# Performance work log

Measured on AMD Instinct MI355X. Metric: run time of the kernel, lower is better.

Reference implementation:

```python
import jax, jax.numpy as jnp
import numpy as np
import math

B, DIM, H, W = 4, 96, 64, 64
DIM3 = DIM * 3
DSTATE = 16

def _dwconv(x, w, b):
    # x: (B, d, L); torch Conv1d(k=4, pad=3, groups=d) then slice [:L] == left-pad 3
    y = jax.lax.conv_general_dilated(x, w, (1,), [(3, 0)],
                                     dimension_numbers=('NCH', 'OIH', 'NCH'),
                                     feature_group_count=x.shape[1])
    return y + b[None, :, None]

def _ln(x, g, b):
    m = jnp.mean(x, -1, keepdims=True)
    v = jnp.var(x, -1, keepdims=True)
    return (x - m) * jax.lax.rsqrt(v + 1e-5) * g + b

def _selective_scan(u, delta, A, Bs, Cs, D, z, delta_bias):
    # u, delta, z: (B, d, L); A: (d, N); Bs, Cs: (B, N, L)
    delta = jax.nn.softplus(delta + delta_bias[None, :, None])
    dT, uT = jnp.moveaxis(delta, 2, 0), jnp.moveaxis(u, 2, 0)   # (L, B, d)
    BT, CT = jnp.moveaxis(Bs, 2, 0), jnp.moveaxis(Cs, 2, 0)     # (L, B, N)
    h0 = jnp.zeros((u.shape[0], A.shape[0], A.shape[1]), u.dtype)
    def step(h, inp):
        d_t, u_t, b_t, c_t = inp
        h = jnp.exp(d_t[..., None] * A) * h + (d_t * u_t)[..., None] * b_t[:, None, :]
        return h, jnp.einsum('bdn,bn->bd', h, c_t)
    _, ys = jax.lax.scan(step, h0, (dT, uT, BT, CT))
    y = jnp.moveaxis(ys, 0, 2) + D[None, :, None] * u
    return y * jax.nn.silu(z)

def _sss(x, z_anchor, in_w, conv_w, conv_b, x_w, dt_w, dt_b, Alog, Dp, out_w):
    Bb, C, Hh, Ww = x.shape
    L = Hh * Ww
    r = dt_w.shape[0]
    xf = x.reshape(Bb, C, L).transpose(0, 2, 1) + z_anchor[:, None, :]
    x_in, z_gate = jnp.split(xf @ in_w, 2, axis=-1)
    xc = jax.nn.silu(_dwconv(x_in.transpose(0, 2, 1), conv_w, conv_b))  # (B, di, L)
    xdbl = xc.transpose(0, 2, 1) @ x_w
    dt, Bs, Cs = jnp.split(xdbl, [r, r + DSTATE], axis=-1)
    y = _selective_scan(xc, (dt @ dt_w).transpose(0, 2, 1), -jnp.exp(Alog),
                        Bs.transpose(0, 2, 1), Cs.transpose(0, 2, 1), Dp,
                        z_gate.transpose(0, 2, 1), dt_b)
    return (y.transpose(0, 2, 1) @ out_w).transpose(0, 2, 1).reshape(Bb, C, Hh, Ww)

def _sts(x, K, Q, in_w, conv_w, conv_b, kln_g, kln_b, k_w, k_b, qln_g, qln_b, q_w, q_b,
         dtbc_w, dt_w, dt_b, gate_w, gate_b, Alog, Dp, out_w):
    Bb, C, Hh, Ww = x.shape
    L = Hh * Ww
    r = dt_w.shape[0]
    xf = x.reshape(Bb, C, L).transpose(0, 2, 1)
    xc = jax.nn.silu(_dwconv((xf @ in_w).transpose(0, 2, 1), conv_w, conv_b))  # (B, di, L)
    x_t = xc.transpose(0, 2, 1)
    Kf = K.reshape(Bb, C, L).transpose(0, 2, 1)
    Qf = Q.reshape(Bb, C, L).transpose(0, 2, 1)
    K_p = jax.nn.silu(_ln(Kf, kln_g, kln_b) @ k_w + k_b)
    Q_p = jax.nn.silu(_ln(Qf, qln_g, qln_b) @ q_w + q_b)
    xdbl = jnp.concatenate([x_t, K_p], -1) @ dtbc_w
    dt, Bs, Cs = jnp.split(xdbl, [r, r + DSTATE], axis=-1)
    z_g = (jnp.concatenate([x_t, Q_p], -1) @ gate_w + gate_b).transpose(0, 2, 1)
    y = _selective_scan(xc, (dt @ dt_w).transpose(0, 2, 1), -jnp.exp(Alog),
                        Bs.transpose(0, 2, 1), Cs.transpose(0, 2, 1), Dp, z_g, dt_b)
    return (y.transpose(0, 2, 1) @ out_w).transpose(0, 2, 1).reshape(Bb, C, Hh, Ww)

def setup_inputs():
    key = jax.random.key(0)
    ks = iter(jax.random.split(key, 64))
    def nrm(shape, s=0.02):
        return jax.random.normal(next(ks), shape, jnp.float32) * s
    di, di3 = DIM * 2, DIM3 * 2
    r, r3 = math.ceil(DIM / 16), math.ceil(DIM3 / 16)
    Alog = jnp.log(jnp.tile(jnp.arange(1.0, DSTATE + 1.0, dtype=jnp.float32), (di, 1)))
    Alog3 = jnp.log(jnp.tile(jnp.arange(1.0, DSTATE + 1.0, dtype=jnp.float32), (di3, 1)))
    return dict(
        m_ll=jax.random.normal(next(ks), (B, DIM, H, W), jnp.float32),
        m_high=jax.random.normal(next(ks), (B, DIM3, H, W), jnp.float32),
        z=jax.random.normal(next(ks), (B, DIM), jnp.float32),
        K=jax.random.normal(next(ks), (B, DIM3, H, W), jnp.float32),
        Q=jax.random.normal(next(ks), (B, DIM3, H, W), jnp.float32),
        s_in_w=nrm((DIM, 2 * di)), s_conv_w=nrm((di, 1, 4), 0.2), s_conv_b=nrm((di,)),
        s_x_w=nrm((di, r + 2 * DSTATE)), s_dt_w=nrm((r, di)), s_dt_b=nrm((di,)),
        s_Alog=Alog, s_D=jnp.ones((di,), jnp.float32), s_out_w=nrm((di, DIM)),
        t_in_w=nrm((DIM3, di3)), t_conv_w=nrm((di3, 1, 4), 0.2), t_conv_b=nrm((di3,)),
        t_kln_g=jnp.ones((DIM3,), jnp.float32), t_kln_b=jnp.zeros((DIM3,), jnp.float32),
        t_k_w=nrm((DIM3, di3)), t_k_b=nrm((di3,)),
        t_qln_g=jnp.ones((DIM3,), jnp.float32), t_qln_b=jnp.zeros((DIM3,), jnp.float32),
        t_q_w=nrm((DIM3, di3)), t_q_b=nrm((di3,)),
        t_dtbc_w=nrm((2 * di3, r3 + 2 * DSTATE)), t_dt_w=nrm((r3, di3)), t_dt_b=nrm((di3,)),
        t_gate_w=nrm((2 * di3, di3)), t_gate_b=nrm((di3,)),
        t_Alog=Alog3, t_D=jnp.ones((di3,), jnp.float32), t_out_w=nrm((di3, DIM3)),
    )

def reference(m_ll, m_high, z, K, Q,
              s_in_w, s_conv_w, s_conv_b, s_x_w, s_dt_w, s_dt_b, s_Alog, s_D, s_out_w,
              t_in_w, t_conv_w, t_conv_b, t_kln_g, t_kln_b, t_k_w, t_k_b,
              t_qln_g, t_qln_b, t_q_w, t_q_b, t_dtbc_w, t_dt_w, t_dt_b,
              t_gate_w, t_gate_b, t_Alog, t_D, t_out_w):
    o1 = m_ll + _sss(m_ll, z, s_in_w, s_conv_w, s_conv_b, s_x_w, s_dt_w, s_dt_b, s_Alog, s_D, s_out_w)
    o2 = m_high + _sts(m_high, K, Q, t_in_w, t_conv_w, t_conv_b, t_kln_g, t_kln_b, t_k_w, t_k_b,
                       t_qln_g, t_qln_b, t_q_w, t_q_b, t_dtbc_w, t_dt_w, t_dt_b,
                       t_gate_w, t_gate_b, t_Alog, t_D, t_out_w)
    return (o1, o2)
```

## Files before the change

### kernel.cpp

```cpp
#include <hip/hip_runtime.h>
#include <math.h>

#define L 4096

typedef unsigned short u16;
typedef float f32x4 __attribute__((ext_vector_type(4)));
typedef short s16x8 __attribute__((ext_vector_type(8)));
typedef __attribute__((address_space(3))) unsigned int lds_u32;
typedef __attribute__((address_space(1))) unsigned int glb_u32;

__device__ __forceinline__ float softplus_f(float x) {
  return fmaxf(x, 0.f) + log1pf(__expf(-fabsf(x)));
}
__device__ __forceinline__ float silu_f(float x) {
  return x / (1.f + __expf(-x));
}
__device__ __forceinline__ float bf2f(u16 v) {
  return __uint_as_float(((unsigned)v) << 16);
}
__device__ __forceinline__ u16 f2bf(float f) {
  unsigned u = __float_as_uint(f);
  u += 0x7FFFu + ((u >> 16) & 1u);
  return (u16)(u >> 16);
}

struct WSeg { const float* src; u16* dst; int K, N, Npad; };
struct WAll { WSeg s[9]; };

__global__ __launch_bounds__(256) void wconv_k(WAll wa) {
  const WSeg w = wa.s[blockIdx.z];
  const int nb = blockIdx.x * 32, kb = blockIdx.y * 32;
  if (nb >= w.Npad || kb >= w.K) return;
  __shared__ float t[32][33];
  const int tx = threadIdx.x & 31, ty = threadIdx.x >> 5;
  for (int r = ty; r < 32; r += 8) {
    int k = kb + r, n = nb + tx;
    t[r][tx] = (n < w.N) ? w.src[(size_t)k * w.N + n] : 0.f;
  }
  __syncthreads();
  for (int r = ty; r < 32; r += 8) {
    int n = nb + r;
    w.dst[(size_t)n * w.K + kb + tx] = f2bf(t[tx][r]);
  }
}

struct TSeg { const float *x, *gam, *bet, *bias2; u16* out; int C, doLN; };
struct TPack { TSeg s[4]; };

__global__ __launch_bounds__(256) void trans_pack_k(TPack pk) {
  const TSeg t = pk.s[blockIdx.x >> 9];
  const int local = blockIdx.x & 511;
  const int C = t.C;
  __shared__ float tile[288][33];
  __shared__ float psum[8][32], psq[8][32];
  __shared__ float mm[32], rr[32];
  const int tid = threadIdx.x;
  const int l0 = (local & 127) * 32;
  const int b = local >> 7;
  const int lane32 = tid & 31, row8 = tid >> 5;
  const float* xb = t.x + (size_t)b * C * L + l0;

  for (int c = row8; c < C; c += 8)
    tile[c][lane32] = xb[(size_t)c * L + lane32];
  __syncthreads();

  if (t.doLN) {
    float s = 0.f, sq = 0.f;
    for (int c = row8; c < C; c += 8) {
      float v = tile[c][lane32];
      s += v; sq = fmaf(v, v, sq);
    }
    psum[row8][lane32] = s; psq[row8][lane32] = sq;
    __syncthreads();
    if (row8 == 0) {
      float ts = 0.f, tq = 0.f;
      #pragma unroll
      for (int g = 0; g < 8; ++g) { ts += psum[g][lane32]; tq += psq[g][lane32]; }
      float m = ts / C;
      float var = tq / C - m * m;
      mm[lane32] = m;
      rr[lane32] = rsqrtf(var + 1e-5f);
    }
    __syncthreads();
  }

  u16* ob = t.out + ((size_t)b * L + l0) * C;
  const int total = 32 * C;
  for (int o = tid * 8; o < total; o += 2048) {
    int tt = o / C, c = o % C;
    float m = 0.f, rs = 0.f;
    if (t.doLN) { m = mm[tt]; rs = rr[tt]; }
    union { u16 u[8]; int4 v; } pkv;
    #pragma unroll
    for (int j = 0; j < 8; ++j) {
      float v = tile[c + j][tt];
      if (t.doLN) v = (v - m) * rs * t.gam[c + j] + t.bet[c + j];
      else if (t.bias2) v += t.bias2[b * C + c + j];
      pkv.u[j] = f2bf(v);
    }
    *(int4*)(ob + o) = pkv.v;
  }
}

struct CSeg { const u16* x; const float* w; const float* b; u16* y; int C, nbx; };
struct CPack { CSeg s[2]; int start1; };

__global__ __launch_bounds__(256) void conv_pack_k(CPack pk) {
  const int bid = blockIdx.x;
  const int si = bid >= pk.start1;
  const CSeg q = pk.s[si];
  const int local = si ? bid - pk.start1 : bid;
  const int C = q.C;
  const int c = (local % q.nbx) * 64 + (threadIdx.x & 63);
  const int chunk = (local / q.nbx) * 4 + (threadIdx.x >> 6);
  const int T0 = chunk * 8;
  const float w0 = q.w[c * 4], w1 = q.w[c * 4 + 1], w2 = q.w[c * 4 + 2], w3 = q.w[c * 4 + 3];
  const float bs = q.b[c];
  const bool first = (T0 & (L - 1)) == 0;
  float v[11];
  #pragma unroll
  for (int i = 0; i < 11; ++i) {
    if (i < 3 && first) v[i] = 0.f;
    else v[i] = bf2f(q.x[(size_t)(T0 - 3 + i) * C + c]);
  }
  #pragma unroll
  for (int j = 0; j < 8; ++j) {
    float s = bs + w0 * v[j] + w1 * v[j + 1] + w2 * v[j + 2] + w3 * v[j + 3];
    q.y[(size_t)(T0 + j) * C + c] = f2bf(silu_f(s));
  }
}

struct MSeg {
  const u16 *A0, *A1, *Wt;
  const float *bias, *res;
  float* outF; u16 *outB0, *outB1;
  int K, K1, Nout, ldA, ldo, split, nbx, nwg, epi;
};
struct MPack { MSeg s[4]; int starts[4]; int nseg; };

__global__ __launch_bounds__(256) void mfma_pack_k(MPack pk) {
  const int bid = blockIdx.x;
  int si = 0;
  #pragma unroll
  for (int k = 1; k < 4; ++k)
    if (k < pk.nseg && bid >= pk.starts[k]) si = k;
  const MSeg p = pk.s[si];
  const int wg = bid - pk.starts[si];

  __shared__ u16 As[2][4096];
  __shared__ u16 Bs[2][4096];
  const int tid = threadIdx.x;
  const int lane = tid & 63;
  const int wid = tid >> 6;
  const int wm = wid >> 1, wn = wid & 1;
  const int newid = (wg & 7) * (p.nwg >> 3) + (wg >> 3);
  const int n0 = (newid % p.nbx) * 128;
  const int m0 = (newid / p.nbx) * 128;
  const int srow = tid & 127;
  const int skc = tid >> 7;
  const int kgrp = lane >> 4, l16 = lane & 15;

  f32x4 acc[4][4];
  #pragma unroll
  for (int i = 0; i < 4; ++i)
    #pragma unroll
    for (int j = 0; j < 4; ++j)
      acc[i][j] = (f32x4){0.f, 0.f, 0.f, 0.f};

  auto stage = [&](int bi, int k0) {
    const u16* Ab = p.A0;
    int kc = k0;
    if (p.A1 && k0 >= p.K1) { Ab = p.A1; kc = k0 - p.K1; }
    const u16* g0 = Ab + (size_t)(m0 + srow) * p.ldA + kc + skc * 8;
    u16* Ad = &As[bi][0];
    __builtin_amdgcn_global_load_lds((const glb_u32*)g0,
        (lds_u32*)(Ad + wid * 512), 16, 0, 0);
    __builtin_amdgcn_global_load_lds((const glb_u32*)(g0 + 16),
        (lds_u32*)(Ad + 2048 + wid * 512), 16, 0, 0);
    const u16* h0 = p.Wt + (size_t)(n0 + srow) * p.K + k0 + skc * 8;
    u16* Bd = &Bs[bi][0];
    __builtin_amdgcn_global_load_lds((const glb_u32*)h0,
        (lds_u32*)(Bd + wid * 512), 16, 0, 0);
    __builtin_amdgcn_global_load_lds((const glb_u32*)(h0 + 16),
        (lds_u32*)(Bd + 2048 + wid * 512), 16, 0, 0);
  };

  const int nt = p.K >> 5;
  stage(0, 0);
  __syncthreads();
  for (int t = 0; t < nt; ++t) {
    const int cur = t & 1;
    if (t + 1 < nt) stage(cur ^ 1, (t + 1) << 5);
    s16x8 af[4], bfr[4];
    #pragma unroll
    for (int mi = 0; mi < 4; ++mi)
      af[mi] = *(const s16x8*)(&As[cur][0] + kgrp * 1024 + (wm * 64 + mi * 16 + l16) * 8);
    #pragma unroll
    for (int ni = 0; ni < 4; ++ni)
      bfr[ni] = *(const s16x8*)(&Bs[cur][0] + kgrp * 1024 + (wn * 64 + ni * 16 + l16) * 8);
    #pragma unroll
    for (int mi = 0; mi < 4; ++mi)
      #pragma unroll
      for (int ni = 0; ni < 4; ++ni)
        acc[mi][ni] = __builtin_amdgcn_mfma_f32_16x16x32_bf16(af[mi], bfr[ni], acc[mi][ni], 0, 0, 0);
    if (t + 1 < nt) __syncthreads();
  }

  if (p.epi == 2) {
    #pragma unroll
    for (int mi = 0; mi < 4; ++mi) {
      int token = m0 + wm * 64 + mi * 16 + (lane >> 4) * 4;
      int b = token >> 12, l = token & (L - 1);
      #pragma unroll
      for (int ni = 0; ni < 4; ++ni) {
        int n = n0 + wn * 64 + ni * 16 + l16;
        if (n < p.Nout) {
          size_t o = ((size_t)b * p.Nout + n) * L + l;
          float4 r = *(const float4*)(p.res + o);
          float4 v = make_float4(acc[mi][ni][0] + r.x, acc[mi][ni][1] + r.y,
                                 acc[mi][ni][2] + r.z, acc[mi][ni][3] + r.w);
          *(float4*)(p.outF + o) = v;
        }
      }
    }
  } else {
    #pragma unroll
    for (int mi = 0; mi < 4; ++mi) {
      #pragma unroll
      for (int j = 0; j < 4; ++j) {
        int token = m0 + wm * 64 + mi * 16 + (lane >> 4) * 4 + j;
        #pragma unroll
        for (int ni = 0; ni < 4; ++ni) {
          int n = n0 + wn * 64 + ni * 16 + l16;
          float v = acc[mi][ni][j];
          if (p.epi == 0) {
            if (n < p.Nout) p.outF[(size_t)token * p.ldo + n] = v;
          } else if (p.epi == 1) {
            if (n < p.Nout) p.outB0[(size_t)token * p.ldo + n] = f2bf(v);
          } else if (p.epi == 3) {
            if (n < p.Nout) p.outB0[(size_t)token * p.ldo + n] = f2bf(silu_f(v + p.bias[n]));
          } else if (p.epi == 4) {
            if (n < p.Nout) p.outB0[(size_t)token * p.ldo + n] = f2bf(v + p.bias[n]);
          } else {
            if (n < p.split) p.outB0[(size_t)token * p.split + n] = f2bf(v);
            else p.outB1[(size_t)token * p.split + (n - p.split)] = f2bf(v);
          }
        }
      }
    }
  }
}

struct FSeg { const float* A0; const float* W; const float* eb; float* out; int K, N, lda, ldo, nbx; };
struct FPack { FSeg s[2]; int start1; };

__global__ __launch_bounds__(256) void gemm_f32_pack_k(FPack pk) {
  const int bid = blockIdx.x;
  const int si = bid >= pk.start1;
  const FSeg p = pk.s[si];
  const int local = si ? bid - pk.start1 : bid;
  const int n0 = (local % p.nbx) * 64;
  const int m0 = (local / p.nbx) * 64;

  __shared__ __align__(16) float As[16][64];
  __shared__ __align__(16) float Bs[16][64];
  const int tid = threadIdx.x;
  const int kidx = tid >> 4;
  const int li4 = (tid & 15) << 2;
  const int r0 = (tid & 15) << 2;
  const int c0 = (tid >> 4) << 2;
  float acc[4][4] = {};

  for (int k0 = 0; k0 < p.K; k0 += 16) {
    __syncthreads();
    {
      const int row = tid >> 2;
      const int kk4 = (tid & 3) << 2;
      const float* src = p.A0 + (size_t)(m0 + row) * p.lda;
      #pragma unroll
      for (int j = 0; j < 4; ++j) {
        int k = k0 + kk4 + j;
        As[kk4 + j][row] = (k < p.K) ? src[k] : 0.f;
      }
    }
    {
      int k = k0 + kidx;
      #pragma unroll
      for (int j = 0; j < 4; ++j) {
        int n = n0 + li4 + j;
        Bs[kidx][li4 + j] = (k < p.K && n < p.N) ? p.W[(size_t)k * p.N + n] : 0.f;
      }
    }
    __syncthreads();
    #pragma unroll
    for (int kk = 0; kk < 16; ++kk) {
      float4 a = *(const float4*)&As[kk][r0];
      float4 bq = *(const float4*)&Bs[kk][c0];
      float av[4] = {a.x, a.y, a.z, a.w};
      float bv[4] = {bq.x, bq.y, bq.z, bq.w};
      #pragma unroll
      for (int i = 0; i < 4; ++i)
        #pragma unroll
        for (int j = 0; j < 4; ++j)
          acc[i][j] = fmaf(av[i], bv[j], acc[i][j]);
    }
  }
  float eb[4] = {p.eb[n0 + c0], p.eb[n0 + c0 + 1], p.eb[n0 + c0 + 2], p.eb[n0 + c0 + 3]};
  #pragma unroll
  for (int i = 0; i < 4; ++i) {
    float4 v;
    v.x = softplus_f(acc[i][0] + eb[0]);
    v.y = softplus_f(acc[i][1] + eb[1]);
    v.z = softplus_f(acc[i][2] + eb[2]);
    v.w = softplus_f(acc[i][3] + eb[3]);
    *(float4*)&p.out[(size_t)(m0 + r0 + i) * p.ldo + n0 + c0] = v;
  }
}

struct SSeg {
  const u16* u; const float* dlt; const float* Alog; const float* xdbl;
  const float* Dp; const u16* zT; float* PF; u16* yT;
  int roff, Dch, CLen, NCH, nxc;
};
struct SPack { SSeg s[2]; int start1; };

template<int PASS>
__global__ __launch_bounds__(64) void scan_pack_k(SPack pk) {
  const int bid = blockIdx.x;
  const int si = bid >= pk.start1;
  const SSeg q = pk.s[si];
  const int local = si ? bid - pk.start1 : bid;
  const int NC = L / q.CLen;
  const int d = (local % q.nxc) * 64 + threadIdx.x;
  const int c = (local / q.nxc) % NC;
  const int b = local / (q.nxc * NC);
  const int Dch = q.Dch;
  const int ch = b * Dch + d;
  const size_t tok0 = (size_t)b * L + (size_t)c * q.CLen;
  float An[16], h[16], P[16];
  #pragma unroll
  for (int n = 0; n < 16; ++n) {
    An[n] = -__expf(q.Alog[d * 16 + n]);
    P[n] = 1.f; h[n] = 0.f;
  }
  if (PASS == 3) {
    #pragma unroll
    for (int n2 = 0; n2 < 16; ++n2)
      h[n2] = q.PF[((size_t)c * 32 + 16 + n2) * q.NCH + ch];
  }
  const float Dd = q.Dp[d];
  const u16* up = q.u + tok0 * Dch + d;
  const float* dp = q.dlt + tok0 * Dch + d;
  const u16* zp = q.zT + tok0 * Dch + d;
  u16* yr = q.yT + tok0 * Dch + d;
  const float* xr = q.xdbl + tok0 * 64 + q.roff;
  for (int t = 0; t < q.CLen; ++t) {
    const size_t od = (size_t)t * Dch;
    float dl = dp[od];
    float uu = bf2f(up[od]);
    float w = dl * uu;
    const float2* bp = (const float2*)(xr + (size_t)t * 64);
    float y = 0.f;
    #pragma unroll
    for (int qq = 0; qq < 8; ++qq) {
      float2 bv = bp[qq];
      float a0 = __expf(dl * An[2 * qq]);
      float a1 = __expf(dl * An[2 * qq + 1]);
      h[2 * qq]     = fmaf(a0, h[2 * qq],     w * bv.x);
      h[2 * qq + 1] = fmaf(a1, h[2 * qq + 1], w * bv.y);
      if (PASS == 1) {
        P[2 * qq] *= a0; P[2 * qq + 1] *= a1;
      } else {
        float2 cv = bp[qq + 8];
        y = fmaf(h[2 * qq], cv.x, y);
        y = fmaf(h[2 * qq + 1], cv.y, y);
      }
    }
    if (PASS == 3) {
      float zv = bf2f(zp[od]);
      yr[od] = f2bf((y + Dd * uu) * silu_f(zv));
    }
  }
  if (PASS == 1) {
    #pragma unroll
    for (int n2 = 0; n2 < 16; ++n2) {
      q.PF[((size_t)c * 32 + n2) * q.NCH + ch] = P[n2];
      q.PF[((size_t)c * 32 + 16 + n2) * q.NCH + ch] = h[n2];
    }
  }
}

__global__ __launch_bounds__(256) void stitch_pack_k(
    float* PF0, int NC0, int NCH0, int tot0,
    float* PF1, int NC1, int NCH1, int tot1) {
  int idx = blockIdx.x * 256 + threadIdx.x;
  float* PF; int NC, NCH;
  if (idx < tot0) { PF = PF0; NC = NC0; NCH = NCH0; }
  else { idx -= tot0; if (idx >= tot1) return; PF = PF1; NC = NC1; NCH = NCH1; }
  int ch = idx % NCH, n = idx / NCH;
  float hin = 0.f;
  for (int c = 0; c < NC; ++c) {
    float* Ps = PF + ((size_t)c * 32 + n) * NCH + ch;
    float* Fs = PF + ((size_t)c * 32 + 16 + n) * NCH + ch;
    float Pv = *Ps, Fv = *Fs;
    *Fs = hin;
    hin = fmaf(Pv, hin, Fv);
  }
}

extern "C" void kernel_launch(void* const* d_in, const int* in_sizes, int n_in,
                              void* d_out, int out_size, void* d_ws, size_t ws_size,
                              hipStream_t stream) {
  const float* m_ll    = (const float*)d_in[0];
  const float* m_high  = (const float*)d_in[1];
  const float* zanc    = (const float*)d_in[2];
  const float* Kin     = (const float*)d_in[3];
  const float* Qin     = (const float*)d_in[4];
  const float* s_in_w  = (const float*)d_in[5];
  const float* s_conv_w= (const float*)d_in[6];
  const float* s_conv_b= (const float*)d_in[7];
  const float* s_x_w   = (const float*)d_in[8];
  const float* s_dt_w  = (const float*)d_in[9];
  const float* s_dt_b  = (const float*)d_in[10];
  const float* s_Alog  = (const float*)d_in[11];
  const float* s_D     = (const float*)d_in[12];
  const float* s_out_w = (const float*)d_in[13];
  const float* t_in_w  = (const float*)d_in[14];
  const float* t_conv_w= (const float*)d_in[15];
  const float* t_conv_b= (const float*)d_in[16];
  const float* t_kln_g = (const float*)d_in[17];
  const float* t_kln_b = (const float*)d_in[18];
  const float* t_k_w   = (const float*)d_in[19];
  const float* t_k_b   = (const float*)d_in[20];
  const float* t_qln_g = (const float*)d_in[21];
  const float* t_qln_b = (const float*)d_in[22];
  const float* t_q_w   = (const float*)d_in[23];
  const float* t_q_b   = (const float*)d_in[24];
  const float* t_dtbc_w= (const float*)d_in[25];
  const float* t_dt_w  = (const float*)d_in[26];
  const float* t_dt_b  = (const float*)d_in[27];
  const float* t_gate_w= (const float*)d_in[28];
  const float* t_gate_b= (const float*)d_in[29];
  const float* t_Alog  = (const float*)d_in[30];
  const float* t_D     = (const float*)d_in[31];
  const float* t_out_w = (const float*)d_in[32];

  float* out1 = (float*)d_out;
  float* out2 = out1 + (size_t)4 * 96 * L;
  float* ws = (float*)d_ws;

  u16* w_sin   = (u16*)(ws + 0);
  u16* w_sx    = (u16*)(ws + 18432);
  u16* w_sout  = (u16*)(ws + 30720);
  u16* w_tin   = (u16*)(ws + 43008);
  u16* w_tk    = (u16*)(ws + 135168);
  u16* w_tq    = (u16*)(ws + 227328);
  u16* w_tdtbc = (u16*)(ws + 319488);
  u16* w_tgate = (u16*)(ws + 393216);
  u16* w_tout  = (u16*)(ws + 761856);

  float* B_ahi  = ws + 872448;
  float* B_aK   = ws + 2052096;
  float* B_aQ   = ws + 3231744;
  float* B_all  = ws + 4411392;
  float* B_xin  = ws + 5197824;
  float* B_zTs  = ws + 6770688;
  float* B_xc   = ws + 8343552;
  float* B_xin3 = ws + 9916416;
  float* B_xc3  = ws + 14635008;
  float* B_kp   = ws + 19353600;
  float* B_qp   = ws + 24072192;
  float* B_zg3  = ws + 28790784;
  float* B_xdbl = ws + 33509376;
  float* B_xdbl3= ws + 34557952;
  float* B_PFs  = ws + 35606528;
  float* B_dlt  = B_ahi;
  float* B_dlt3 = B_kp;
  u16* y_bf = (u16*)B_xin;
  u16* y3   = (u16*)B_xin3;
  float* PFt = out2;

  dim3 blk(256);

  {
    WAll wa;
    wa.s[0] = {s_in_w,   w_sin,    96, 384, 384};
    wa.s[1] = {s_x_w,    w_sx,    192,  38, 128};
    wa.s[2] = {s_out_w,  w_sout,  192,  96, 128};
    wa.s[3] = {t_in_w,   w_tin,   288, 576, 640};
    wa.s[4] = {t_k_w,    w_tk,    288, 576, 640};
    wa.s[5] = {t_q_w,    w_tq,    288, 576, 640};
    wa.s[6] = {t_dtbc_w, w_tdtbc, 1152, 50, 128};
    wa.s[7] = {t_gate_w, w_tgate, 1152, 576, 640};
    wa.s[8] = {t_out_w,  w_tout,  576, 288, 384};
    wconv_k<<<dim3(20, 36, 9), blk, 0, stream>>>(wa);
  }

  {
    TPack tp{};
    tp.s[0] = {m_ll,   nullptr, nullptr, zanc,    (u16*)B_all, 96,  0};
    tp.s[1] = {m_high, nullptr, nullptr, nullptr, (u16*)B_ahi, 288, 0};
    tp.s[2] = {Kin,    t_kln_g, t_kln_b, nullptr, (u16*)B_aK,  288, 1};
    tp.s[3] = {Qin,    t_qln_g, t_qln_b, nullptr, (u16*)B_aQ,  288, 1};
    trans_pack_k<<<dim3(2048), blk, 0, stream>>>(tp);
  }

  {
    MPack pk{}; pk.nseg = 4;
    pk.starts[0] = 0; pk.starts[1] = 384; pk.starts[2] = 1024; pk.starts[3] = 1664;
    MSeg a{}; a.A0 = (u16*)B_all; a.Wt = w_sin; a.K = 96; a.K1 = 1 << 28; a.Nout = 384;
    a.ldA = 96; a.split = 192; a.outB0 = (u16*)B_xin; a.outB1 = (u16*)B_zTs;
    a.nbx = 3; a.nwg = 384; a.epi = 5; pk.s[0] = a;
    MSeg b{}; b.A0 = (u16*)B_ahi; b.Wt = w_tin; b.K = 288; b.K1 = 1 << 28; b.Nout = 576;
    b.ldA = 288; b.ldo = 576; b.outB0 = (u16*)B_xin3; b.nbx = 5; b.nwg = 640; b.epi = 1; pk.s[1] = b;
    MSeg c{}; c.A0 = (u16*)B_aK; c.Wt = w_tk; c.K = 288; c.K1 = 1 << 28; c.Nout = 576;
    c.ldA = 288; c.ldo = 576; c.bias = t_k_b; c.outB0 = (u16*)B_kp; c.nbx = 5; c.nwg = 640; c.epi = 3; pk.s[2] = c;
    MSeg d{}; d.A0 = (u16*)B_aQ; d.Wt = w_tq; d.K = 288; d.K1 = 1 << 28; d.Nout = 576;
    d.ldA = 288; d.ldo = 576; d.bias = t_q_b; d.outB0 = (u16*)B_qp; d.nbx = 5; d.nwg = 640; d.epi = 3; pk.s[3] = d;
    mfma_pack_k<<<dim3(2304), blk, 0, stream>>>(pk);
  }

  {
    CPack cp{}; cp.start1 = 1536;
    cp.s[0] = {(u16*)B_xin,  s_conv_w, s_conv_b, (u16*)B_xc,  192, 3};
    cp.s[1] = {(u16*)B_xin3, t_conv_w, t_conv_b, (u16*)B_xc3, 576, 9};
    conv_pack_k<<<dim3(6144), blk, 0, stream>>>(cp);
  }

  {
    MPack pk{}; pk.nseg = 3;
    pk.starts[0] = 0; pk.starts[1] = 128; pk.starts[2] = 256; pk.starts[3] = 896;
    MSeg a{}; a.A0 = (u16*)B_xc; a.Wt = w_sx; a.K = 192; a.K1 = 1 << 28; a.Nout = 64;
    a.ldA = 192; a.ldo = 64; a.outF = B_xdbl; a.nbx = 1; a.nwg = 128; a.epi = 0; pk.s[0] = a;
    MSeg b{}; b.A0 = (u16*)B_xc3; b.A1 = (u16*)B_kp; b.Wt = w_tdtbc; b.K = 1152; b.K1 = 576;
    b.Nout = 64; b.ldA = 576; b.ldo = 64; b.outF = B_xdbl3; b.nbx = 1; b.nwg = 128; b.epi = 0; pk.s[1] = b;
    MSeg c{}; c.A0 = (u16*)B_xc3; c.A1 = (u16*)B_qp; c.Wt = w_tgate; c.K = 1152; c.K1 = 576;
    c.Nout = 576; c.ldA = 576; c.ldo = 576; c.bias = t_gate_b; c.outB0 = (u16*)B_zg3;
    c.nbx = 5; c.nwg = 640; c.epi = 4; pk.s[2] = c;
    mfma_pack_k<<<dim3(896), blk, 0, stream>>>(pk);
  }

  {
    FPack fp{}; fp.start1 = 768;
    fp.s[0] = {B_xdbl,  s_dt_w, s_dt_b, B_dlt,  6,  192, 64, 192, 3};
    fp.s[1] = {B_xdbl3, t_dt_w, t_dt_b, B_dlt3, 18, 576, 64, 576, 9};
    gemm_f32_pack_k<<<dim3(3072), blk, 0, stream>>>(fp);
  }

  SPack sp{}; sp.start1 = 1536;
  sp.s[0] = {(u16*)B_xc,  B_dlt,  s_Alog, B_xdbl,  s_D, (u16*)B_zTs, B_PFs, y_bf, 6,  192, 32, 768,  3};
  sp.s[1] = {(u16*)B_xc3, B_dlt3, t_Alog, B_xdbl3, t_D, (u16*)B_zg3, PFt,   y3,   18, 576, 64, 2304, 9};
  scan_pack_k<1><<<dim3(3840), dim3(64), 0, stream>>>(sp);
  stitch_pack_k<<<dim3(192), blk, 0, stream>>>(B_PFs, 128, 768, 12288, PFt, 64, 2304, 36864);
  scan_pack_k<3><<<dim3(3840), dim3(64), 0, stream>>>(sp);

  {
    MPack pk{}; pk.nseg = 2;
    pk.starts[0] = 0; pk.starts[1] = 128; pk.starts[2] = 512; pk.starts[3] = 512;
    MSeg a{}; a.A0 = y_bf; a.Wt = w_sout; a.K = 192; a.K1 = 1 << 28; a.Nout = 96;
    a.ldA = 192; a.res = m_ll; a.outF = out1; a.nbx = 1; a.nwg = 128; a.epi = 2; pk.s[0] = a;
    MSeg b{}; b.A0 = y3; b.Wt = w_tout; b.K = 576; b.K1 = 1 << 28; b.Nout = 288;
    b.ldA = 576; b.res = m_high; b.outF = out2; b.nbx = 3; b.nwg = 384; b.epi = 2; pk.s[1] = b;
    mfma_pack_k<<<dim3(512), blk, 0, stream>>>(pk);
  }
}
```

Measured before the change: 476.3 us.

## Scan two channels per thread and use power-structured A for exp reuse

The selective scan kernel now handles two adjacent channels per thread, using vectorized loads and stores for delta, u, z and y, in 256-thread blocks. When Alog gives A[n] ≈ (n+1)·A[0], which holds for the standard S4D-real initialization, it computes one exp per step and forms the rest by repeated multiplication instead of 16 exps. Pass 1 now gets the chunk decay product as exp(A·sum(delta)) rather than a running product. The repeated multiplication may accumulate rounding error, the fast path relies on a property of the parameter values checked at runtime, and doubling state registers may reduce occupancy.

```diff
diff --git a/kernel.cpp b/kernel.cpp
--- a/kernel.cpp
+++ b/kernel.cpp
@@ -4,6 +4,7 @@
 #define L 4096
 
 typedef unsigned short u16;
+typedef unsigned int u32;
 typedef float f32x4 __attribute__((ext_vector_type(4)));
 typedef short s16x8 __attribute__((ext_vector_type(8)));
 typedef __attribute__((address_space(3))) unsigned int lds_u32;
@@ -317,75 +318,122 @@
   }
 }
 
-struct SSeg {
+struct S2Seg {
   const u16* u; const float* dlt; const float* Alog; const float* xdbl;
   const float* Dp; const u16* zT; float* PF; u16* yT;
-  int roff, Dch, CLen, NCH, nxc;
+  int roff, Dch, CLen, NCH;
 };
-struct SPack { SSeg s[2]; int start1; };
+struct S2Pack { S2Seg s[2]; int start1; };
 
 template<int PASS>
-__global__ __launch_bounds__(64) void scan_pack_k(SPack pk) {
+__global__ __launch_bounds__(256) void scan2_pack_k(S2Pack pk) {
   const int bid = blockIdx.x;
   const int si = bid >= pk.start1;
-  const SSeg q = pk.s[si];
-  const int local = si ? bid - pk.start1 : bid;
+  const S2Seg q = pk.s[si];
+  const int lbid = si ? bid - pk.start1 : bid;
+  const int gtid = lbid * 256 + (int)threadIdx.x;
+  const int Dch = q.Dch;
+  const int npair = Dch >> 1;
   const int NC = L / q.CLen;
-  const int d = (local % q.nxc) * 64 + threadIdx.x;
-  const int c = (local / q.nxc) % NC;
-  const int b = local / (q.nxc * NC);
-  const int Dch = q.Dch;
-  const int ch = b * Dch + d;
+  const int dpi = gtid % npair;
+  const int c = (gtid / npair) % NC;
+  const int b = gtid / (npair * NC);
+  const int d0 = dpi * 2;
   const size_t tok0 = (size_t)b * L + (size_t)c * q.CLen;
-  float An[16], h[16], P[16];
+
+  float An[2][16], h[2][16];
   #pragma unroll
-  for (int n = 0; n < 16; ++n) {
-    An[n] = -__expf(q.Alog[d * 16 + n]);
-    P[n] = 1.f; h[n] = 0.f;
-  }
+  for (int j = 0; j < 2; ++j)
+    #pragma unroll
+    for (int n = 0; n < 16; ++n) {
+      An[j][n] = -__expf(q.Alog[(d0 + j) * 16 + n]);
+      h[j][n] = 0.f;
+    }
+  bool fast = true;
+  #pragma unroll
+  for (int j = 0; j < 2; ++j)
+    #pragma unroll
+    for (int n = 1; n < 16; ++n) {
+      float ref = (float)(n + 1) * An[j][0];
+      if (fabsf(An[j][n] - ref) > 1e-4f * fabsf(ref)) fast = false;
+    }
+
+  const int ch0 = b * Dch + d0;
   if (PASS == 3) {
     #pragma unroll
-    for (int n2 = 0; n2 < 16; ++n2)
-      h[n2] = q.PF[((size_t)c * 32 + 16 + n2) * q.NCH + ch];
-  }
-  const float Dd = q.Dp[d];
-  const u16* up = q.u + tok0 * Dch + d;
-  const float* dp = q.dlt + tok0 * Dch + d;
-  const u16* zp = q.zT + tok0 * Dch + d;
-  u16* yr = q.yT + tok0 * Dch + d;
+    for (int j = 0; j < 2; ++j)
+      #pragma unroll
+      for (int n = 0; n < 16; ++n)
+        h[j][n] = q.PF[((size_t)c * 32 + 16 + n) * q.NCH + ch0 + j];
+  }
+  const float Dd0 = q.Dp[d0], Dd1 = q.Dp[d0 + 1];
+  const u16* up = q.u + tok0 * Dch + d0;
+  const float* dp = q.dlt + tok0 * Dch + d0;
+  const u16* zp = q.zT + tok0 * Dch + d0;
+  u16* yr = q.yT + tok0 * Dch + d0;
   const float* xr = q.xdbl + tok0 * 64 + q.roff;
-  for (int t = 0; t < q.CLen; ++t) {
-    const size_t od = (size_t)t * Dch;
-    float dl = dp[od];
-    float uu = bf2f(up[od]);
-    float w = dl * uu;
-    const float2* bp = (const float2*)(xr + (size_t)t * 64);
-    float y = 0.f;
-    #pragma unroll
-    for (int qq = 0; qq < 8; ++qq) {
-      float2 bv = bp[qq];
-      float a0 = __expf(dl * An[2 * qq]);
-      float a1 = __expf(dl * An[2 * qq + 1]);
-      h[2 * qq]     = fmaf(a0, h[2 * qq],     w * bv.x);
-      h[2 * qq + 1] = fmaf(a1, h[2 * qq + 1], w * bv.y);
-      if (PASS == 1) {
-        P[2 * qq] *= a0; P[2 * qq + 1] *= a1;
-      } else {
-        float2 cv = bp[qq + 8];
-        y = fmaf(h[2 * qq], cv.x, y);
-        y = fmaf(h[2 * qq + 1], cv.y, y);
-      }
-    }
-    if (PASS == 3) {
-      float zv = bf2f(zp[od]);
-      yr[od] = f2bf((y + Dd * uu) * silu_f(zv));
-    }
-  }
+  float S0 = 0.f, S1 = 0.f;
+
+  #define SCAN_BODY(FAST)                                                      \
+  for (int t = 0; t < q.CLen; ++t) {                                           \
+    const size_t od = (size_t)t * Dch;                                         \
+    float2 dl2 = *(const float2*)(dp + od);                                    \
+    u32 uu2 = *(const u32*)(up + od);                                          \
+    float u0 = bf2f((u16)uu2), u1 = bf2f((u16)(uu2 >> 16));                    \
+    float w0 = dl2.x * u0, w1 = dl2.y * u1;                                    \
+    const float2* bp = (const float2*)(xr + (size_t)t * 64);                   \
+    float Bv[16];                                                              \
+    _Pragma("unroll")                                                          \
+    for (int qq = 0; qq < 8; ++qq) {                                           \
+      float2 bv = bp[qq]; Bv[2 * qq] = bv.x; Bv[2 * qq + 1] = bv.y;            \
+    }                                                                          \
+    if (PASS == 1) { S0 += dl2.x; S1 += dl2.y; }                               \
+    float y0 = 0.f, y1 = 0.f;                                                  \
+    if (FAST) {                                                                \
+      float a0 = __expf(dl2.x * An[0][0]);                                     \
+      float a1 = __expf(dl2.y * An[1][0]);                                     \
+      float e0 = a0, e1 = a1;                                                  \
+      h[0][0] = fmaf(e0, h[0][0], w0 * Bv[0]);                                 \
+      h[1][0] = fmaf(e1, h[1][0], w1 * Bv[0]);                                 \
+      _Pragma("unroll")                                                        \
+      for (int n = 1; n < 16; ++n) {                                           \
+        e0 *= a0; e1 *= a1;                                                    \
+        h[0][n] = fmaf(e0, h[0][n], w0 * Bv[n]);                               \
+        h[1][n] = fmaf(e1, h[1][n], w1 * Bv[n]);                               \
+      }                                                                        \
+    } else {                                                                   \
+      _Pragma("unroll")                                                        \
+      for (int n = 0; n < 16; ++n) {                                           \
+        h[0][n] = fmaf(__expf(dl2.x * An[0][n]), h[0][n], w0 * Bv[n]);         \
+        h[1][n] = fmaf(__expf(dl2.y * An[1][n]), h[1][n], w1 * Bv[n]);         \
+      }                                                                        \
+    }                                                                          \
+    if (PASS == 3) {                                                           \
+      _Pragma("unroll")                                                        \
+      for (int qq = 0; qq < 8; ++qq) {                                         \
+        float2 cv = bp[qq + 8];                                                \
+        y0 = fmaf(h[0][2 * qq], cv.x, y0); y0 = fmaf(h[0][2 * qq + 1], cv.y, y0); \
+        y1 = fmaf(h[1][2 * qq], cv.x, y1); y1 = fmaf(h[1][2 * qq + 1], cv.y, y1); \
+      }                                                                        \
+      u32 zz2 = *(const u32*)(zp + od);                                        \
+      float z0 = bf2f((u16)zz2), z1 = bf2f((u16)(zz2 >> 16));                  \
+      y0 = (y0 + Dd0 * u0) * silu_f(z0);                                       \
+      y1 = (y1 + Dd1 * u1) * silu_f(z1);                                       \
+      u32 out = (u32)f2bf(y0) | ((u32)f2bf(y1) << 16);                         \
+      *(u32*)(yr + od) = out;                                                  \
+    }                                                                          \
+  }
+
+  if (fast) { SCAN_BODY(1) } else { SCAN_BODY(0) }
+  #undef SCAN_BODY
+
   if (PASS == 1) {
     #pragma unroll
-    for (int n2 = 0; n2 < 16; ++n2) {
-      q.PF[((size_t)c * 32 + n2) * q.NCH + ch] = P[n2];
-      q.PF[((size_t)c * 32 + 16 + n2) * q.NCH + ch] = h[n2];
+    for (int n = 0; n < 16; ++n) {
+      q.PF[((size_t)c * 32 + n) * q.NCH + ch0]     = __expf(An[0][n] * S0);
+      q.PF[((size_t)c * 32 + n) * q.NCH + ch0 + 1] = __expf(An[1][n] * S1);
+      q.PF[((size_t)c * 32 + 16 + n) * q.NCH + ch0]     = h[0][n];
+      q.PF[((size_t)c * 32 + 16 + n) * q.NCH + ch0 + 1] = h[1][n];
     }
   }
 }
@@ -547,12 +595,12 @@
     gemm_f32_pack_k<<<dim3(3072), blk, 0, stream>>>(fp);
   }
 
-  SPack sp{}; sp.start1 = 1536;
-  sp.s[0] = {(u16*)B_xc,  B_dlt,  s_Alog, B_xdbl,  s_D, (u16*)B_zTs, B_PFs, y_bf, 6,  192, 32, 768,  3};
-  sp.s[1] = {(u16*)B_xc3, B_dlt3, t_Alog, B_xdbl3, t_D, (u16*)B_zg3, PFt,   y3,   18, 576, 64, 2304, 9};
-  scan_pack_k<1><<<dim3(3840), dim3(64), 0, stream>>>(sp);
+  S2Pack sp{}; sp.start1 = 192;
+  sp.s[0] = {(u16*)B_xc,  B_dlt,  s_Alog, B_xdbl,  s_D, (u16*)B_zTs, B_PFs, y_bf, 6,  192, 32, 768};
+  sp.s[1] = {(u16*)B_xc3, B_dlt3, t_Alog, B_xdbl3, t_D, (u16*)B_zg3, PFt,   y3,   18, 576, 64, 2304};
+  scan2_pack_k<1><<<dim3(480), blk, 0, stream>>>(sp);
   stitch_pack_k<<<dim3(192), blk, 0, stream>>>(B_PFs, 128, 768, 12288, PFt, 64, 2304, 36864);
-  scan_pack_k<3><<<dim3(3840), dim3(64), 0, stream>>>(sp);
+  scan2_pack_k<3><<<dim3(480), blk, 0, stream>>>(sp);
 
   {
     MPack pk{}; pk.nseg = 2;
```

New measurement: 428.8 us. 10.0% less time.
